# Kernel optimization log

Hardware: AMD Instinct MI355X
Metric: run time of the kernel (lower is better)

The kernel has to match this reference:

```python
import jax, jax.numpy as jnp
import numpy as np

IMG = 800.0
OUT = 7          # output_size
SR = 2           # sampling_ratio
SCALES = (0.25, 0.125, 0.0625, 0.03125)  # FPN strides 4,8,16,32
CANON_SCALE = 224.0
CANON_LVL = 4.0
K_MIN, K_MAX = 2.0, 5.0  # -log2(scales[0]), -log2(scales[-1])
EPS = 1e-6


def setup_inputs() -> dict:
    key = jax.random.key(0)
    k0, k1, k2, k3, kp = jax.random.split(key, 5)
    feat0 = jax.random.normal(k0, (2, 256, 200, 200), dtype=jnp.float32)
    feat1 = jax.random.normal(k1, (2, 256, 100, 100), dtype=jnp.float32)
    feat2 = jax.random.normal(k2, (2, 256, 50, 50), dtype=jnp.float32)
    feat3 = jax.random.normal(k3, (2, 256, 25, 25), dtype=jnp.float32)
    # two random corner points per box, sorted so x0<=x1, y0<=y1
    pts = jax.random.uniform(kp, (2, 512, 2, 2), dtype=jnp.float32) * IMG
    proposals = jnp.concatenate([pts.min(axis=2), pts.max(axis=2)], axis=-1)  # [B,N,4] = x0,y0,x1,y1
    return {"feat0": feat0, "feat1": feat1, "feat2": feat2, "feat3": feat3,
            "proposals": proposals}


def _roi_align(feat, bidx, boxes, scale):
    """torchvision roi_align (aligned=False) for all boxes on one feature map.
    feat: [B,C,H,W], bidx: [N] int32 image index, boxes: [N,4] image coords.
    Returns [N,C,OUT,OUT]."""
    H, W = feat.shape[2], feat.shape[3]
    x0 = boxes[:, 0] * scale
    y0 = boxes[:, 1] * scale
    x1 = boxes[:, 2] * scale
    y1 = boxes[:, 3] * scale
    roi_w = jnp.maximum(x1 - x0, 1.0)
    roi_h = jnp.maximum(y1 - y0, 1.0)
    bin_w = roi_w / OUT
    bin_h = roi_h / OUT
    # sample offsets within the roi, in bin units: [OUT*SR]
    off = (jnp.arange(OUT, dtype=jnp.float32)[:, None]
           + (jnp.arange(SR, dtype=jnp.float32)[None, :] + 0.5) / SR).reshape(-1)
    ys = y0[:, None] + off[None, :] * bin_h[:, None]  # [N, OUT*SR]
    xs = x0[:, None] + off[None, :] * bin_w[:, None]  # [N, OUT*SR]

    def prep(c, size):
        valid = (c >= -1.0) & (c <= float(size))
        cc = jnp.maximum(c, 0.0)
        lo0 = jnp.floor(cc).astype(jnp.int32)
        at_edge = lo0 >= size - 1
        lo = jnp.where(at_edge, size - 1, lo0)
        hi = jnp.where(at_edge, size - 1, lo0 + 1)
        frac = jnp.where(at_edge, 0.0, cc - lo0.astype(cc.dtype))
        return lo, hi, frac, valid

    yl, yh, ly, vy = prep(ys, H)
    xl, xh, lx, vx = prep(xs, W)
    hy, hx = 1.0 - ly, 1.0 - lx
    b3 = bidx[:, None, None]

    def gather(yi, xi):
        # advanced indices (b, y, x) with channel slice -> [N, Sy, Sx, C]
        return feat[b3, :, yi[:, :, None], xi[:, None, :]]

    val = ((hy[:, :, None] * hx[:, None, :])[..., None] * gather(yl, xl)
           + (hy[:, :, None] * lx[:, None, :])[..., None] * gather(yl, xh)
           + (ly[:, :, None] * hx[:, None, :])[..., None] * gather(yh, xl)
           + (ly[:, :, None] * lx[:, None, :])[..., None] * gather(yh, xh))
    mask = (vy[:, :, None] & vx[:, None, :]).astype(val.dtype)[..., None]
    val = val * mask
    N, C = boxes.shape[0], feat.shape[1]
    val = val.reshape(N, OUT, SR, OUT, SR, C).mean(axis=(2, 4))  # avg over samples
    return val.transpose(0, 3, 1, 2)  # [N, C, OUT, OUT]


def reference(feat0, feat1, feat2, feat3, proposals):
    feats = (feat0, feat1, feat2, feat3)
    B, Np = proposals.shape[0], proposals.shape[1]
    boxes = proposals.reshape(-1, 4)                      # [N,4]
    bidx = jnp.repeat(jnp.arange(B, dtype=jnp.int32), Np)  # image id per roi
    # LevelMapper: FPN paper heuristic
    areas = (boxes[:, 2] - boxes[:, 0]) * (boxes[:, 3] - boxes[:, 1])
    s = jnp.sqrt(areas)
    lvls = jnp.floor(CANON_LVL + jnp.log2(s / CANON_SCALE + EPS))
    lvls = (jnp.clip(lvls, K_MIN, K_MAX) - K_MIN).astype(jnp.int32)  # 0..3
    N, C = boxes.shape[0], feat0.shape[1]
    result = jnp.zeros((N, C, OUT, OUT), dtype=feat0.dtype)
    for l, (feat, scale) in enumerate(zip(feats, SCALES)):
        pooled = _roi_align(feat, bidx, boxes, scale)
        result = result + jnp.where((lvls == l)[:, None, None, None], pooled, 0.0)
    return result
```

## Files before the change

### kernel.cpp

```cpp
#include <hip/hip_runtime.h>
#include <hip/hip_fp16.h>
#include <math.h>

#define POUT 7
#define NCH 256

#define HW0 40000
#define HW1 10000
#define HW2 2500
#define HW3 625
#define WS_OFF0 0
#define WS_OFF1 (2*NCH*HW0)
#define WS_OFF2 (WS_OFF1 + 2*NCH*HW1)
#define WS_OFF3 (WS_OFF2 + 2*NCH*HW2)
#define WS_ELEMS (WS_OFF3 + 2*NCH*HW3)
#define WS_PERM_OFF (WS_ELEMS + 256)
#define WS_NEED  ((size_t)(WS_PERM_OFF + 1024) * sizeof(float))

#define TP 56
#define RS 114
#define NT0 ((HW0 + TP - 1) / TP)
#define NT1 ((HW1 + TP - 1) / TP)
#define NT2 ((HW2 + TP - 1) / TP)
#define NT3 ((HW3 + TP - 1) / TP)
#define NBLK ((NT0 + NT1 + NT2 + NT3) * 4)

__global__ __launch_bounds__(512, 8) void transpose_fused_kernel(
    const float* __restrict__ f0, const float* __restrict__ f1,
    const float* __restrict__ f2, const float* __restrict__ f3,
    float* __restrict__ ws, const float* __restrict__ props,
    int boxes_per_img, int N)
{
    __shared__ float tile[64 * RS];

    const int gid = blockIdx.x;
    int id = gid;
    const float* src; int HW, nt; size_t woff;
    if (id < NT0 * 4)                        { src = f0; HW = HW0; nt = NT0; woff = WS_OFF0; }
    else if ((id -= NT0 * 4) < NT1 * 4)      { src = f1; HW = HW1; nt = NT1; woff = WS_OFF1; }
    else if ((id -= NT1 * 4) < NT2 * 4)      { src = f2; HW = HW2; nt = NT2; woff = WS_OFF2; }
    else { id -= NT2 * 4;                      src = f3; HW = HW3; nt = NT3; woff = WS_OFF3; }

    const int ch = id & 1;
    const int tl = (id >> 1) % nt;
    const int bb = (id >> 1) / nt;
    const int p0 = tl * TP;
    const int pn = min(TP, HW - p0);
    const int c0 = ch * 128;
    const int t  = threadIdx.x;

    const float* sbase = src + ((size_t)(bb * NCH + c0)) * HW + p0;

    if (pn == TP) {
        for (int i = t; i < 128 * (TP / 4); i += 512) {
            const int c  = i / (TP / 4);
            const int p4 = i - c * (TP / 4);
            const float4 v = *(const float4*)&sbase[(size_t)c * HW + p4 * 4];
            float* d = &tile[(c >> 1) * RS + (c & 1) + p4 * 8];
            d[0] = v.x; d[2] = v.y; d[4] = v.z; d[6] = v.w;
        }
    } else {
        for (int i = t; i < 128 * (TP / 4); i += 512) {
            const int c  = i / (TP / 4);
            const int pb = (i - c * (TP / 4)) * 4;
            float vv[4];
            #pragma unroll
            for (int k = 0; k < 4; ++k)
                vv[k] = (pb + k < pn) ? sbase[(size_t)c * HW + pb + k] : 0.0f;
            float* d = &tile[(c >> 1) * RS + (c & 1) + pb * 2];
            d[0] = vv[0]; d[2] = vv[1]; d[4] = vv[2]; d[6] = vv[3];
        }
    }
    __syncthreads();

    float* dbase = ws + woff + ((size_t)bb * HW + p0) * NCH + c0;
    for (int i = t; i < 64 * TP; i += 512) {
        const int c2 = i & 63, p = i >> 6;
        if (p < pn) {
            const float2 v = *(const float2*)&tile[c2 * RS + 2 * p];
            *(float2*)&dbase[(size_t)p * NCH + 2 * c2] = v;
        }
    }

    if (gid == 0) {
        __syncthreads();
        unsigned* keys = (unsigned*)tile;
        if (N == 1024) {
            for (int i = t; i < 1024; i += 512) {
                const float4 box = ((const float4*)props)[i];
                const float area = (box.z - box.x) * (box.w - box.y);
                float lvlf = floorf(4.0f + log2f(sqrtf(area) / 224.0f + 1e-6f));
                lvlf = fminf(fmaxf(lvlf, 2.0f), 5.0f) - 2.0f;
                const int l = (int)lvlf;
                const float sc = 0.25f / (float)(1 << l);
                int yc = (int)(0.5f * (box.y + box.w) * sc);
                int xc = (int)(0.5f * (box.x + box.z) * sc);
                yc = yc < 0 ? 0 : (yc > 255 ? 255 : yc);
                xc = xc < 0 ? 0 : (xc > 255 ? 255 : xc);
                const unsigned hi = (unsigned)((i / boxes_per_img) * 4 + l);
                keys[i] = (((hi << 8 | (unsigned)yc) << 8 | (unsigned)xc) << 10) | (unsigned)i;
            }
            for (int size = 2; size <= 1024; size <<= 1)
                for (int stride = size >> 1; stride > 0; stride >>= 1) {
                    __syncthreads();
                    const int lo = t & (stride - 1);
                    const int k  = ((t ^ lo) << 1) | lo;
                    const unsigned a = keys[k], b2 = keys[k + stride];
                    if ((a > b2) == ((k & size) == 0)) { keys[k] = b2; keys[k + stride] = a; }
                }
            __syncthreads();
            int* perm = (int*)(ws + WS_PERM_OFF);
            for (int i = t; i < 1024; i += 512) perm[i] = (int)(keys[i] & 1023u);
        }
        if (t < 256) ws[WS_ELEMS + t] = 0.0f;
    }
}

__global__ __launch_bounds__(256, 4) void roi_gather_kernel(
    const float* __restrict__ ws, const float* __restrict__ props,
    float* __restrict__ out, int boxes_per_img)
{
    __shared__ int4  sRec[196];
    __shared__ float sStage[64 * 49];

    const int* perm = (const int*)(ws + WS_PERM_OFF);
    const int n = perm[(blockIdx.x & 7) * 128 + (blockIdx.x >> 3)];
    const int t = threadIdx.x;
    const int b = n / boxes_per_img;

    const float4 box = ((const float4*)props)[n];
    const float area = (box.z - box.x) * (box.w - box.y);
    float lvlf = floorf(4.0f + log2f(sqrtf(area) / 224.0f + 1e-6f));
    lvlf = fminf(fmaxf(lvlf, 2.0f), 5.0f) - 2.0f;
    const int l = (int)lvlf;

    int sz; size_t lvl_off;
    if      (l == 0) { sz = 200; lvl_off = WS_OFF0; }
    else if (l == 1) { sz = 100; lvl_off = WS_OFF1; }
    else if (l == 2) { sz = 50;  lvl_off = WS_OFF2; }
    else             { sz = 25;  lvl_off = WS_OFF3; }
    const int HW = sz * sz;
    const float scale = 0.25f / (float)(1 << l);

    if (t < 196) {
        const int bin = t >> 2, sub = t & 3;
        const int ph = bin / POUT, pw = bin % POUT;
        const int iy = sub >> 1,  ix = sub & 1;

        const float x0 = box.x * scale, y0 = box.y * scale;
        const float x1 = box.z * scale, y1 = box.w * scale;
        const float bin_w = fmaxf(x1 - x0, 1.0f) / (float)POUT;
        const float bin_h = fmaxf(y1 - y0, 1.0f) / (float)POUT;

        const float ys = y0 + ((float)ph + ((float)iy + 0.5f) * 0.5f) * bin_h;
        const float xs = x0 + ((float)pw + ((float)ix + 0.5f) * 0.5f) * bin_w;

        const bool  vy  = (ys >= -1.0f) && (ys <= (float)sz);
        const float cy  = fmaxf(ys, 0.0f);
        const int   yl0 = (int)floorf(cy);
        const bool  ey  = yl0 >= sz - 1;
        const int   yl  = ey ? sz - 1 : yl0;
        const int   yh  = ey ? sz - 1 : yl0 + 1;
        const float ly  = ey ? 0.0f : cy - (float)yl0;

        const bool  vx  = (xs >= -1.0f) && (xs <= (float)sz);
        const float cx  = fmaxf(xs, 0.0f);
        const int   xl0 = (int)floorf(cx);
        const bool  ex  = xl0 >= sz - 1;
        const int   xl  = ex ? sz - 1 : xl0;
        const float lx  = ex ? 0.0f : cx - (float)xl0;

        const float hy = 1.0f - ly, hx = 1.0f - lx;
        const float m  = (vy && vx) ? 0.25f : 0.0f;
        const float w00 = hy * hx * m, w01 = hy * lx * m;
        const float w10 = ly * hx * m, w11 = ly * lx * m;

        __half2 p01 = __floats2half2_rn(w00, w01);
        __half2 p23 = __floats2half2_rn(w10, w11);

        int4 rec;
        rec.x = (yl * sz + xl) * NCH;
        rec.y = *reinterpret_cast<const int*>(&p01);
        rec.z = *reinterpret_cast<const int*>(&p23);
        rec.w = (yh * sz + xl) * NCH;
        sRec[t] = rec;
    }
    __syncthreads();

    const float* fb = ws + lvl_off + (size_t)b * (size_t)HW * NCH + t;

    float acc[49];
    #pragma unroll
    for (int bin = 0; bin < 49; ++bin) {
        float a = 0.0f;
        #pragma unroll
        for (int sub = 0; sub < 4; ++sub) {
            const int4 rec = sRec[bin * 4 + sub];
            const __half2 h01 = *reinterpret_cast<const __half2*>(&rec.y);
            const __half2 h23 = *reinterpret_cast<const __half2*>(&rec.z);
            const float2 w01 = __half22float2(h01);
            const float2 w23 = __half22float2(h23);
            a += w01.x * fb[rec.x] + w01.y * fb[rec.x + NCH]
               + w23.x * fb[rec.w] + w23.y * fb[rec.w + NCH];
        }
        acc[bin] = a;
    }

    __syncthreads();
    float* obase = out + (size_t)n * (NCH * 49);
    #pragma unroll
    for (int r = 0; r < 4; ++r) {
        if ((t >> 6) == r) {
            #pragma unroll
            for (int i = 0; i < 49; ++i) sStage[(t & 63) * 49 + i] = acc[i];
        }
        __syncthreads();
        float4* d4 = (float4*)(obase + r * (64 * 49));
        const float4* s4 = (const float4*)sStage;
        for (int i = t; i < 64 * 49 / 4; i += 256) d4[i] = s4[i];
        __syncthreads();
    }
}

__global__ __launch_bounds__(256, 4) void roi_align_nchw_kernel(
    const float* __restrict__ f0, const float* __restrict__ f1,
    const float* __restrict__ f2, const float* __restrict__ f3,
    const float* __restrict__ props, float* __restrict__ out, int boxes_per_img)
{
    const int n = blockIdx.x;
    const int t = threadIdx.x;
    if (t >= 196) return;
    const int bin = t >> 2, q = t & 3;
    const int ph = bin / POUT, pw = bin % POUT;
    const int iy = q >> 1,    ix = q & 1;
    const int b = n / boxes_per_img;

    const float4 box = ((const float4*)props)[n];
    const float area = (box.z - box.x) * (box.w - box.y);
    float lvlf = floorf(4.0f + log2f(sqrtf(area) / 224.0f + 1e-6f));
    lvlf = fminf(fmaxf(lvlf, 2.0f), 5.0f) - 2.0f;
    const int l = (int)lvlf;

    const float* feat; int sz;
    if      (l == 0) { feat = f0; sz = 200; }
    else if (l == 1) { feat = f1; sz = 100; }
    else if (l == 2) { feat = f2; sz = 50;  }
    else             { feat = f3; sz = 25;  }
    const float scale = 0.25f / (float)(1 << l);

    const float x0 = box.x * scale, y0 = box.y * scale;
    const float x1 = box.z * scale, y1 = box.w * scale;
    const float bin_w = fmaxf(x1 - x0, 1.0f) / (float)POUT;
    const float bin_h = fmaxf(y1 - y0, 1.0f) / (float)POUT;
    const float ysamp = y0 + ((float)ph + ((float)iy + 0.5f) * 0.5f) * bin_h;
    const float xsamp = x0 + ((float)pw + ((float)ix + 0.5f) * 0.5f) * bin_w;

    const bool  vy  = (ysamp >= -1.0f) && (ysamp <= (float)sz);
    const float cy  = fmaxf(ysamp, 0.0f);
    const int   yl0 = (int)floorf(cy);
    const bool  ey  = yl0 >= sz - 1;
    const int   yl  = ey ? sz - 1 : yl0;
    const int   yh  = ey ? sz - 1 : yl0 + 1;
    const float ly  = ey ? 0.0f : cy - (float)yl0;
    const bool  vx  = (xsamp >= -1.0f) && (xsamp <= (float)sz);
    const float cx  = fmaxf(xsamp, 0.0f);
    const int   xl0 = (int)floorf(cx);
    const bool  ex  = xl0 >= sz - 1;
    const int   xl  = ex ? sz - 1 : xl0;
    const int   xh  = ex ? sz - 1 : xl0 + 1;
    const float lx  = ex ? 0.0f : cx - (float)xl0;

    const float hy = 1.0f - ly, hx = 1.0f - lx;
    const float m  = (vy && vx) ? 1.0f : 0.0f;
    const float w00 = hy * hx * m, w01 = hy * lx * m;
    const float w10 = ly * hx * m, w11 = ly * lx * m;

    const int HW = sz * sz;
    const float* base = feat + (size_t)b * NCH * HW;
    int o00 = yl * sz + xl, o01 = yl * sz + xh;
    int o10 = yh * sz + xl, o11 = yh * sz + xh;
    float* op = out + (size_t)n * NCH * (POUT * POUT) + bin;

    #pragma unroll 4
    for (int cch = 0; cch < NCH; ++cch) {
        float v = w00 * base[o00] + w01 * base[o01]
                + w10 * base[o10] + w11 * base[o11];
        v += __shfl_xor(v, 1);
        v += __shfl_xor(v, 2);
        if (q == 0) op[cch * (POUT * POUT)] = v * 0.25f;
        o00 += HW; o01 += HW; o10 += HW; o11 += HW;
    }
}

extern "C" void kernel_launch(void* const* d_in, const int* in_sizes, int n_in,
                              void* d_out, int out_size, void* d_ws, size_t ws_size,
                              hipStream_t stream) {
    const float* f0 = (const float*)d_in[0];
    const float* f1 = (const float*)d_in[1];
    const float* f2 = (const float*)d_in[2];
    const float* f3 = (const float*)d_in[3];
    const float* props = (const float*)d_in[4];
    float* out = (float*)d_out;

    const int N = in_sizes[4] / 4;
    const int B = in_sizes[0] / (NCH * HW0);
    const int boxes_per_img = N / B;

    if (ws_size >= WS_NEED && B == 2 && N == 1024) {
        float* wsf = (float*)d_ws;
        transpose_fused_kernel<<<NBLK, 512, 0, stream>>>(f0, f1, f2, f3, wsf,
                                                         props, boxes_per_img, N);
        roi_gather_kernel<<<N, 256, 0, stream>>>(wsf, props, out, boxes_per_img);
    } else {
        roi_align_nchw_kernel<<<N, 256, 0, stream>>>(f0, f1, f2, f3, props, out, boxes_per_img);
    }
}
```

Baseline: 223.5 us.

## Store transposed feature workspace in fp16 and split gather across channel pairs

```diff
diff --git a/kernel.cpp b/kernel.cpp
--- a/kernel.cpp
+++ b/kernel.cpp
@@ -4,6 +4,8 @@
 
 #define POUT 7
 #define NCH 256
+
+typedef float v4f __attribute__((ext_vector_type(4)));
 
 #define HW0 40000
 #define HW1 10000
@@ -14,8 +16,9 @@
 #define WS_OFF2 (WS_OFF1 + 2*NCH*HW1)
 #define WS_OFF3 (WS_OFF2 + 2*NCH*HW2)
 #define WS_ELEMS (WS_OFF3 + 2*NCH*HW3)
-#define WS_PERM_OFF (WS_ELEMS + 256)
-#define WS_NEED  ((size_t)(WS_PERM_OFF + 1024) * sizeof(float))
+#define WS_SLACK 512
+#define WS_PERM_BYTE ((size_t)(WS_ELEMS + WS_SLACK) * 2)
+#define WS_NEED (WS_PERM_BYTE + 1024 * sizeof(int))
 
 #define TP 56
 #define RS 114
@@ -28,7 +31,7 @@
 __global__ __launch_bounds__(512, 8) void transpose_fused_kernel(
     const float* __restrict__ f0, const float* __restrict__ f1,
     const float* __restrict__ f2, const float* __restrict__ f3,
-    float* __restrict__ ws, const float* __restrict__ props,
+    __half* __restrict__ ws, const float* __restrict__ props,
     int boxes_per_img, int N)
 {
     __shared__ float tile[64 * RS];
@@ -55,9 +58,10 @@
         for (int i = t; i < 128 * (TP / 4); i += 512) {
             const int c  = i / (TP / 4);
             const int p4 = i - c * (TP / 4);
-            const float4 v = *(const float4*)&sbase[(size_t)c * HW + p4 * 4];
+            const v4f v = __builtin_nontemporal_load(
+                (const v4f*)&sbase[(size_t)c * HW + p4 * 4]);
             float* d = &tile[(c >> 1) * RS + (c & 1) + p4 * 8];
-            d[0] = v.x; d[2] = v.y; d[4] = v.z; d[6] = v.w;
+            d[0] = v[0]; d[2] = v[1]; d[4] = v[2]; d[6] = v[3];
         }
     } else {
         for (int i = t; i < 128 * (TP / 4); i += 512) {
@@ -73,12 +77,12 @@
     }
     __syncthreads();
 
-    float* dbase = ws + woff + ((size_t)bb * HW + p0) * NCH + c0;
+    __half* dbase = ws + woff + ((size_t)bb * HW + p0) * NCH + c0;
     for (int i = t; i < 64 * TP; i += 512) {
         const int c2 = i & 63, p = i >> 6;
         if (p < pn) {
             const float2 v = *(const float2*)&tile[c2 * RS + 2 * p];
-            *(float2*)&dbase[(size_t)p * NCH + 2 * c2] = v;
+            *(__half2*)&dbase[(size_t)p * NCH + 2 * c2] = __floats2half2_rn(v.x, v.y);
         }
     }
 
@@ -109,30 +113,30 @@
                     if ((a > b2) == ((k & size) == 0)) { keys[k] = b2; keys[k + stride] = a; }
                 }
             __syncthreads();
-            int* perm = (int*)(ws + WS_PERM_OFF);
-            for (int i = t; i < 1024; i += 512) perm[i] = (int)(keys[i] & 1023u);
-        }
-        if (t < 256) ws[WS_ELEMS + t] = 0.0f;
+            int* perm = (int*)((char*)ws + WS_PERM_BYTE);
+            for (int i = t; i < 1024; i += 512) {
+                const unsigned k = keys[i];
+                perm[i] = (int)((k & 1023u) | (((k >> 26) & 3u) << 10) | ((k >> 28) << 12));
+            }
+        }
+        if (t < 256) ((unsigned*)(ws + WS_ELEMS))[t] = 0u;
     }
 }
 
 __global__ __launch_bounds__(256, 4) void roi_gather_kernel(
-    const float* __restrict__ ws, const float* __restrict__ props,
+    const __half* __restrict__ ws, const float* __restrict__ props,
     float* __restrict__ out, int boxes_per_img)
 {
-    __shared__ int4  sRec[196];
-    __shared__ float sStage[64 * 49];
-
-    const int* perm = (const int*)(ws + WS_PERM_OFF);
-    const int n = perm[(blockIdx.x & 7) * 128 + (blockIdx.x >> 3)];
+    __shared__ int2   sOff[196];
+    __shared__ float4 sW[196];
+    __shared__ __align__(16) float sStage[64 * 49];
+
+    const int* perm = (const int*)((const char*)ws + WS_PERM_BYTE);
+    const int pe = perm[(blockIdx.x & 7) * 128 + (blockIdx.x >> 3)];
+    const int n = pe & 1023;
+    const int l = (pe >> 10) & 3;
+    const int b = pe >> 12;
     const int t = threadIdx.x;
-    const int b = n / boxes_per_img;
-
-    const float4 box = ((const float4*)props)[n];
-    const float area = (box.z - box.x) * (box.w - box.y);
-    float lvlf = floorf(4.0f + log2f(sqrtf(area) / 224.0f + 1e-6f));
-    lvlf = fminf(fmaxf(lvlf, 2.0f), 5.0f) - 2.0f;
-    const int l = (int)lvlf;
 
     int sz; size_t lvl_off;
     if      (l == 0) { sz = 200; lvl_off = WS_OFF0; }
@@ -143,6 +147,7 @@
     const float scale = 0.25f / (float)(1 << l);
 
     if (t < 196) {
+        const float4 box = ((const float4*)props)[n];
         const int bin = t >> 2, sub = t & 3;
         const int ph = bin / POUT, pw = bin % POUT;
         const int iy = sub >> 1,  ix = sub & 1;
@@ -172,52 +177,61 @@
 
         const float hy = 1.0f - ly, hx = 1.0f - lx;
         const float m  = (vy && vx) ? 0.25f : 0.0f;
-        const float w00 = hy * hx * m, w01 = hy * lx * m;
-        const float w10 = ly * hx * m, w11 = ly * lx * m;
-
-        __half2 p01 = __floats2half2_rn(w00, w01);
-        __half2 p23 = __floats2half2_rn(w10, w11);
-
-        int4 rec;
-        rec.x = (yl * sz + xl) * NCH;
-        rec.y = *reinterpret_cast<const int*>(&p01);
-        rec.z = *reinterpret_cast<const int*>(&p23);
-        rec.w = (yh * sz + xl) * NCH;
-        sRec[t] = rec;
+        sOff[t] = make_int2((yl * sz + xl) * NCH, (yh * sz + xl) * NCH);
+        sW[t]   = make_float4(hy * hx * m, hy * lx * m, ly * hx * m, ly * lx * m);
     }
     __syncthreads();
 
-    const float* fb = ws + lvl_off + (size_t)b * (size_t)HW * NCH + t;
-
-    float acc[49];
+    const int c2 = t & 127;
+    const int hf = t >> 7;
+    const int bin0 = hf * 24;
+    const __half* fb = ws + lvl_off + (size_t)b * (size_t)HW * NCH + 2 * c2;
+
+    float2 acc[25];
     #pragma unroll
-    for (int bin = 0; bin < 49; ++bin) {
-        float a = 0.0f;
+    for (int j = 0; j < 25; ++j) { acc[j].x = 0.0f; acc[j].y = 0.0f; }
+
+    #pragma unroll
+    for (int j = 0; j < 25; ++j) {
+        const int rbase = (bin0 + j) * 4;
         #pragma unroll
-        for (int sub = 0; sub < 4; ++sub) {
-            const int4 rec = sRec[bin * 4 + sub];
-            const __half2 h01 = *reinterpret_cast<const __half2*>(&rec.y);
-            const __half2 h23 = *reinterpret_cast<const __half2*>(&rec.z);
-            const float2 w01 = __half22float2(h01);
-            const float2 w23 = __half22float2(h23);
-            a += w01.x * fb[rec.x] + w01.y * fb[rec.x + NCH]
-               + w23.x * fb[rec.w] + w23.y * fb[rec.w + NCH];
-        }
-        acc[bin] = a;
+        for (int s = 0; s < 4; ++s) {
+            const int2   o = sOff[rbase + s];
+            const float4 w = sW[rbase + s];
+            const float2 v00 = __half22float2(*(const __half2*)&fb[o.x]);
+            const float2 v01 = __half22float2(*(const __half2*)&fb[o.x + NCH]);
+            const float2 v10 = __half22float2(*(const __half2*)&fb[o.y]);
+            const float2 v11 = __half22float2(*(const __half2*)&fb[o.y + NCH]);
+            acc[j].x += w.x * v00.x + w.y * v01.x + w.z * v10.x + w.w * v11.x;
+            acc[j].y += w.x * v00.y + w.y * v01.y + w.z * v10.y + w.w * v11.y;
+        }
     }
 
     __syncthreads();
     float* obase = out + (size_t)n * (NCH * 49);
     #pragma unroll
     for (int r = 0; r < 4; ++r) {
-        if ((t >> 6) == r) {
-            #pragma unroll
-            for (int i = 0; i < 49; ++i) sStage[(t & 63) * 49 + i] = acc[i];
+        if ((c2 >> 5) == r) {
+            const int lc = (c2 & 31) * 2;
+            if (hf == 0) {
+                #pragma unroll
+                for (int j = 0; j < 25; ++j) {
+                    sStage[lc * 49 + j]       = acc[j].x;
+                    sStage[(lc + 1) * 49 + j] = acc[j].y;
+                }
+            } else {
+                #pragma unroll
+                for (int j = 1; j < 25; ++j) {
+                    sStage[lc * 49 + 24 + j]       = acc[j].x;
+                    sStage[(lc + 1) * 49 + 24 + j] = acc[j].y;
+                }
+            }
         }
         __syncthreads();
-        float4* d4 = (float4*)(obase + r * (64 * 49));
-        const float4* s4 = (const float4*)sStage;
-        for (int i = t; i < 64 * 49 / 4; i += 256) d4[i] = s4[i];
+        v4f* d4 = (v4f*)(obase + r * (64 * 49));
+        const v4f* s4 = (const v4f*)sStage;
+        for (int i = t; i < 64 * 49 / 4; i += 256)
+            __builtin_nontemporal_store(s4[i], &d4[i]);
         __syncthreads();
     }
 }
@@ -307,10 +321,10 @@
     const int boxes_per_img = N / B;
 
     if (ws_size >= WS_NEED && B == 2 && N == 1024) {
-        float* wsf = (float*)d_ws;
-        transpose_fused_kernel<<<NBLK, 512, 0, stream>>>(f0, f1, f2, f3, wsf,
+        __half* wsh = (__half*)d_ws;
+        transpose_fused_kernel<<<NBLK, 512, 0, stream>>>(f0, f1, f2, f3, wsh,
                                                          props, boxes_per_img, N);
-        roi_gather_kernel<<<N, 256, 0, stream>>>(wsf, props, out, boxes_per_img);
+        roi_gather_kernel<<<N, 256, 0, stream>>>(wsh, props, out, boxes_per_img);
     } else {
         roi_align_nchw_kernel<<<N, 256, 0, stream>>>(f0, f1, f2, f3, props, out, boxes_per_img);
     }
```

Measured after the change: 192.0 us. -14.1%, faster.
